# Kernel optimization log

Hardware: AMD Instinct MI355X
Metric: run time of the kernel (lower is better)

## Reference

```python
import jax, jax.numpy as jnp
import numpy as np

N_NODES = 100000
C = 128
E = 800000
V = 50000
NEG_SLOPE = 0.2


def gat_conv(x, edges, W, att_src, att_dst, bias, num_nodes):
    """Single-head PyG-style GATConv with self-loops added (PyG default).

    edges: [2, E] with row 0 = source j, row 1 = destination i.
    """
    loops = jnp.arange(num_nodes, dtype=edges.dtype)
    src = jnp.concatenate([edges[0], loops])  # [E+N]
    dst = jnp.concatenate([edges[1], loops])

    h = x @ W.T                               # [N, C] linear transform
    a_s = h @ att_src                         # [N] per-node src score
    a_d = h @ att_dst                         # [N] per-node dst score

    e = jax.nn.leaky_relu(a_s[src] + a_d[dst], NEG_SLOPE)  # [E+N]
    # scatter-softmax over edges grouped by destination node
    m = jax.ops.segment_max(e, dst, num_segments=num_nodes)
    ex = jnp.exp(e - m[dst])
    denom = jax.ops.segment_sum(ex, dst, num_segments=num_nodes)
    alpha = ex / (denom[dst] + 1e-16)         # [E+N]

    out = jax.ops.segment_sum(alpha[:, None] * h[src], dst, num_segments=num_nodes)
    return out + bias


def setup_inputs() -> dict:
    key = jax.random.key(0)
    ks = jax.random.split(key, 12)
    s = 1.0 / np.sqrt(C)
    return {
        "embedding": jax.random.normal(ks[0], (N_NODES, C), jnp.float32),
        "W1": jax.random.normal(ks[1], (C, C), jnp.float32) * s,
        "att_src1": jax.random.normal(ks[2], (C,), jnp.float32) * s,
        "att_dst1": jax.random.normal(ks[3], (C,), jnp.float32) * s,
        "b1": jax.random.normal(ks[4], (C,), jnp.float32) * s,
        "W2": jax.random.normal(ks[5], (C, C), jnp.float32) * s,
        "att_src2": jax.random.normal(ks[6], (C,), jnp.float32) * s,
        "att_dst2": jax.random.normal(ks[7], (C,), jnp.float32) * s,
        "b2": jax.random.normal(ks[8], (C,), jnp.float32) * s,
        "edges1": jax.random.randint(ks[9], (2, E), 0, N_NODES, jnp.int64 if jax.config.jax_enable_x64 else jnp.int32),
        "edges2": jax.random.randint(ks[10], (2, E), 0, N_NODES, jnp.int64 if jax.config.jax_enable_x64 else jnp.int32),
        "idx_mapping": jax.random.randint(ks[11], (V,), 0, N_NODES, jnp.int64 if jax.config.jax_enable_x64 else jnp.int32),
    }


def reference(embedding, W1, att_src1, att_dst1, b1, W2, att_src2, att_dst2, b2,
              edges1, edges2, idx_mapping):
    h = gat_conv(embedding, edges1, W1, att_src1, att_dst1, b1, N_NODES)
    h = gat_conv(h, edges2, W2, att_src2, att_dst2, b2, N_NODES)
    return h[idx_mapping]
```

## Files before the change

### kernel.cpp

```cpp
#include <hip/hip_runtime.h>

#define N_NODES 100000
#define C_DIM 128
#define E_EDGES 800000
#define V_OUT 50000
#define EN (E_EDGES + N_NODES)
#define M2 (2 * N_NODES)
#define EN2 (2 * EN)

#define BSHIFT 9
#define NBUCK_L ((N_NODES + 511) >> 9)
#define NBUCK2 (2 * NBUCK_L)
#define CAP 8192
#define P1_CHUNK 4096
#define P1_PER_T (P1_CHUNK / 256)
#define NCHUNK ((EN2 + P1_CHUNK - 1) / P1_CHUNK)
#define VFLAG_BLKS ((V_OUT + 255) / 256)

#define XPAD 136
#define LDS_E 768

#define NCHUNKS_G ((N_NODES + 63) / 64)
#define GEMM_GRID 512

typedef unsigned int uint;
typedef unsigned short ushort;
typedef __attribute__((ext_vector_type(8))) short bf16x8;
typedef __attribute__((ext_vector_type(4))) float f32x4;

static __device__ __forceinline__ ushort f2bf(float f) {
    uint u = __float_as_uint(f);
    u += 0x7fffu + ((u >> 16) & 1);
    return (ushort)(u >> 16);
}

template <int IN_F32>
__global__ __launch_bounds__(256) void gemm_mfma(
    const void* __restrict__ xin, const float* __restrict__ W,
    const float* __restrict__ att_s, const float* __restrict__ att_d,
    ushort* __restrict__ hb, float* __restrict__ a_s, float* __restrict__ a_d)
{
    __shared__ ushort ws[128 * XPAD];
    __shared__ ushort xs[2][64 * XPAD];
    const int tid = threadIdx.x;

    {
        const int row = tid >> 1, half = tid & 1;
        const float* src = W + row * 128 + half * 64;
        ushort* dst = &ws[row * XPAD + half * 64];
        #pragma unroll
        for (int i = 0; i < 8; ++i) {
            float4 u = *reinterpret_cast<const float4*>(src + i * 8);
            float4 v = *reinterpret_cast<const float4*>(src + i * 8 + 4);
            uint4 pk;
            pk.x = (uint)f2bf(u.x) | ((uint)f2bf(u.y) << 16);
            pk.y = (uint)f2bf(u.z) | ((uint)f2bf(u.w) << 16);
            pk.z = (uint)f2bf(v.x) | ((uint)f2bf(v.y) << 16);
            pk.w = (uint)f2bf(v.z) | ((uint)f2bf(v.w) << 16);
            *reinterpret_cast<uint4*>(dst + i * 8) = pk;
        }
    }

    const int srow_t = tid >> 2, q = tid & 3;
    const int lane = tid & 63, wv = tid >> 6;
    const int m = lane & 15, quad = lane >> 4;

    int c = blockIdx.x;
    float4 pf_f[8];
    uint4  pf_b[4];

    {
        const long srow = min((long)c * 64 + srow_t, (long)N_NODES - 1);
        if (IN_F32) {
            const float* src = (const float*)xin + srow * 128 + q * 32;
            #pragma unroll
            for (int i = 0; i < 8; ++i)
                pf_f[i] = *reinterpret_cast<const float4*>(src + i * 4);
        } else {
            const ushort* src = (const ushort*)xin + srow * 128 + q * 32;
            #pragma unroll
            for (int i = 0; i < 4; ++i)
                pf_b[i] = *reinterpret_cast<const uint4*>(src + i * 8);
        }
        ushort* dst = &xs[0][srow_t * XPAD + q * 32];
        if (IN_F32) {
            #pragma unroll
            for (int i = 0; i < 4; ++i) {
                uint4 pk;
                pk.x = (uint)f2bf(pf_f[2*i].x)   | ((uint)f2bf(pf_f[2*i].y)   << 16);
                pk.y = (uint)f2bf(pf_f[2*i].z)   | ((uint)f2bf(pf_f[2*i].w)   << 16);
                pk.z = (uint)f2bf(pf_f[2*i+1].x) | ((uint)f2bf(pf_f[2*i+1].y) << 16);
                pk.w = (uint)f2bf(pf_f[2*i+1].z) | ((uint)f2bf(pf_f[2*i+1].w) << 16);
                *reinterpret_cast<uint4*>(dst + i * 8) = pk;
            }
        } else {
            #pragma unroll
            for (int i = 0; i < 4; ++i)
                *reinterpret_cast<uint4*>(dst + i * 8) = pf_b[i];
        }
    }
    __syncthreads();

    int cur = 0;
    while (c < NCHUNKS_G) {
        const int cn = c + GEMM_GRID;

        if (cn < NCHUNKS_G) {
            const long srow = min((long)cn * 64 + srow_t, (long)N_NODES - 1);
            if (IN_F32) {
                const float* src = (const float*)xin + srow * 128 + q * 32;
                #pragma unroll
                for (int i = 0; i < 8; ++i)
                    pf_f[i] = *reinterpret_cast<const float4*>(src + i * 4);
            } else {
                const ushort* src = (const ushort*)xin + srow * 128 + q * 32;
                #pragma unroll
                for (int i = 0; i < 4; ++i)
                    pf_b[i] = *reinterpret_cast<const uint4*>(src + i * 8);
            }
        }

        const int n0 = c * 64 + wv * 16;
        bf16x8 a[4];
        #pragma unroll
        for (int ki = 0; ki < 4; ++ki)
            a[ki] = *reinterpret_cast<const bf16x8*>(&xs[cur][(wv*16+m)*XPAD + quad*8 + ki*32]);
        __syncthreads();

        float ps[4] = {0, 0, 0, 0}, pd[4] = {0, 0, 0, 0};
        #pragma unroll
        for (int ct = 0; ct < 8; ++ct) {
            const int cc = ct * 16 + m;
            f32x4 acc = {0.f, 0.f, 0.f, 0.f};
            #pragma unroll
            for (int ki = 0; ki < 4; ++ki) {
                bf16x8 b = *reinterpret_cast<const bf16x8*>(&ws[cc*XPAD + quad*8 + ki*32]);
                acc = __builtin_amdgcn_mfma_f32_16x16x32_bf16(a[ki], b, acc, 0, 0, 0);
            }
            const float asc = att_s[cc], adc = att_d[cc];
            #pragma unroll
            for (int r = 0; r < 4; ++r) {
                xs[cur][(wv*16 + quad*4 + r) * XPAD + cc] = f2bf(acc[r]);
                ps[r] = fmaf(acc[r], asc, ps[r]);
                pd[r] = fmaf(acc[r], adc, pd[r]);
            }
        }
        __syncthreads();

        {
            const int sub = tid & 15, rb = tid >> 4;
            #pragma unroll
            for (int i = 0; i < 4; ++i) {
                const int rl = rb + i * 16;
                const int node = c * 64 + rl;
                uint4 v = *reinterpret_cast<const uint4*>(&xs[cur][rl * XPAD + sub * 8]);
                if (node < N_NODES)
                    *reinterpret_cast<uint4*>(hb + (long)node * 128 + sub * 8) = v;
            }
        }
        #pragma unroll
        for (int r = 0; r < 4; ++r) {
            float s = ps[r], d = pd[r];
            #pragma unroll
            for (int x = 1; x < 16; x <<= 1) { s += __shfl_xor(s, x); d += __shfl_xor(d, x); }
            const int node = n0 + quad * 4 + r;
            if (m == 0 && node < N_NODES) { a_s[node] = s; a_d[node] = d; }
        }

        if (cn < NCHUNKS_G) {
            ushort* dst = &xs[cur ^ 1][srow_t * XPAD + q * 32];
            if (IN_F32) {
                #pragma unroll
                for (int i = 0; i < 4; ++i) {
                    uint4 pk;
                    pk.x = (uint)f2bf(pf_f[2*i].x)   | ((uint)f2bf(pf_f[2*i].y)   << 16);
                    pk.y = (uint)f2bf(pf_f[2*i].z)   | ((uint)f2bf(pf_f[2*i].w)   << 16);
                    pk.z = (uint)f2bf(pf_f[2*i+1].x) | ((uint)f2bf(pf_f[2*i+1].y) << 16);
                    pk.w = (uint)f2bf(pf_f[2*i+1].z) | ((uint)f2bf(pf_f[2*i+1].w) << 16);
                    *reinterpret_cast<uint4*>(dst + i * 8) = pk;
                }
            } else {
                #pragma unroll
                for (int i = 0; i < 4; ++i)
                    *reinterpret_cast<uint4*>(dst + i * 8) = pf_b[i];
            }
        }
        __syncthreads();
        cur ^= 1;
        c = cn;
    }
}

__global__ __launch_bounds__(256) void partition_kernel(
    const int* __restrict__ e1, const int* __restrict__ e2,
    int* __restrict__ cursor, uint* __restrict__ slab,
    const int* __restrict__ idxm, int* __restrict__ head, int* __restrict__ nextp)
{
    __shared__ int cnt[NBUCK2];
    __shared__ int basearr[NBUCK2];
    const int tid = threadIdx.x;
    const int blk = blockIdx.x;
    if (blk >= NCHUNK) {
        int v = (blk - NCHUNK) * 256 + tid;
        if (v < V_OUT) {
            int n = idxm[v];
            int old = atomicExch(&head[n], v);
            nextp[v] = old;
        }
        return;
    }
    for (int i = tid; i < NBUCK2; i += 256) cnt[i] = 0;
    __syncthreads();

    const int e0 = blk * P1_CHUNK;
    uint ent[P1_PER_T];
    int  bkt[P1_PER_T];
    #pragma unroll
    for (int i = 0; i < P1_PER_T; ++i) {
        int e = e0 + i * 256 + tid;
        bkt[i] = -1;
        if (e < EN2) {
            int src, dst, lb;
            if (e < EN) {
                if (e < E_EDGES) { src = e1[e]; dst = e1[E_EDGES + e]; }
                else             { src = dst = e - E_EDGES; }
                lb = 0;
            } else {
                int f = e - EN;
                if (f < E_EDGES) { src = e2[f]; dst = e2[E_EDGES + f]; }
                else             { src = dst = f - E_EDGES; }
                lb = NBUCK_L;
            }
            bkt[i] = lb + (dst >> BSHIFT);
            ent[i] = (uint)src | ((uint)(dst & 511) << 17);
            atomicAdd(&cnt[bkt[i]], 1);
        }
    }
    __syncthreads();
    for (int b = tid; b < NBUCK2; b += 256) {
        int c = cnt[b];
        basearr[b] = (c > 0) ? atomicAdd(&cursor[b], c) : 0;
        cnt[b] = 0;
    }
    __syncthreads();
    #pragma unroll
    for (int i = 0; i < P1_PER_T; ++i) {
        if (bkt[i] >= 0) {
            int r = basearr[bkt[i]] + atomicAdd(&cnt[bkt[i]], 1);
            if (r < CAP) slab[(long)bkt[i] * CAP + r] = ent[i];
        }
    }
}

__global__ __launch_bounds__(256) void local_csr(
    const uint* __restrict__ slab, const int* __restrict__ cursor,
    int* __restrict__ offs, uint* __restrict__ esrc)
{
    __shared__ uint ent[CAP];
    __shared__ int deg[512];
    __shared__ int excl[512];
    __shared__ int sbase;
    const int b = blockIdx.x;
    const int tid = threadIdx.x;
    const int cnt = min(cursor[b], CAP);
    const int layer = (b >= NBUCK_L);
    const int node0 = (b - layer * NBUCK_L) << BSHIFT;
    const int obase = layer * N_NODES;
    const int nodes_n = min(512, N_NODES - node0);

    for (int i = tid; i < 512; i += 256) deg[i] = 0;
    if (tid < 64) {
        int s = 0;
        #pragma unroll
        for (int k = 0; k < 7; ++k) {
            int idx = tid + 64 * k;
            if (idx < b) s += cursor[idx];
        }
        #pragma unroll
        for (int d = 32; d > 0; d >>= 1) s += __shfl_down(s, d);
        if (tid == 0) sbase = s;
    }
    __syncthreads();
    const int base = sbase;

    for (int i = tid; i < cnt; i += 256) {
        uint v = slab[(long)b * CAP + i];
        ent[i] = v;
        atomicAdd(&deg[v >> 17], 1);
    }
    __syncthreads();
    if (tid < 64) {
        int v8[8]; int s = 0;
        #pragma unroll
        for (int i = 0; i < 8; ++i) { v8[i] = deg[tid * 8 + i]; s += v8[i]; }
        int incl = s;
        #pragma unroll
        for (int d = 1; d < 64; d <<= 1) {
            int t = __shfl_up(incl, d);
            if (tid >= d) incl += t;
        }
        int e = incl - s;
        #pragma unroll
        for (int i = 0; i < 8; ++i) { excl[tid * 8 + i] = e; e += v8[i]; }
    }
    __syncthreads();
    for (int i = tid; i < nodes_n; i += 256)
        offs[obase + node0 + i] = base + excl[i];
    for (int i = tid; i < 512; i += 256) deg[i] = 0;
    if (tid == 0 && node0 + 512 >= N_NODES)
        offs[obase + N_NODES] = base + cnt;
    __syncthreads();
    for (int i = tid; i < cnt; i += 256) {
        uint v = ent[i];
        int dl = v >> 17;
        int r = atomicAdd(&deg[dl], 1);
        esrc[base + excl[dl] + r] = v;
    }
}

template <int MODE>
__global__ __launch_bounds__(256) void aggregate(
    const ushort* __restrict__ hb, const float* __restrict__ a_s,
    const float* __restrict__ a_d, const float* __restrict__ bias,
    const int* __restrict__ offs, const uint* __restrict__ esrc,
    const int* __restrict__ head, const int* __restrict__ nextp,
    void* __restrict__ outp, int obase)
{
    __shared__ uint2 ew[LDS_E];
    const int tid = threadIdx.x;
    const int node0 = blockIdx.x * 16;
    const int bnode0 = (node0 >> BSHIFT) << BSHIFT;
    const int bstart = offs[obase + node0];
    const int bend   = offs[obase + node0 + 16];
    const int nE = bend - bstart;

    for (int i = tid; i < min(nE, LDS_E); i += 256) {
        uint v = esrc[bstart + i];
        float w = 0.0f;
        const int d = bnode0 + (v >> 17);
        if (MODE == 0 || head[d] >= 0) {
            float e = a_s[v & 0x1ffff] + a_d[d];
            e = (e >= 0.0f) ? e : 0.2f * e;
            w = __expf(e);
        }
        ew[i] = make_uint2(v, __float_as_uint(w));
    }
    __syncthreads();

    const int wave = tid >> 6;
    const int lane = tid & 63;
    const int slot = lane >> 4;
    const int c16  = lane & 15;
    const int node = node0 + wave * 4 + slot;
    int hv = 0;
    if (MODE == 1) {
        hv = head[node];
        if (hv < 0) return;
    }

    const int start = offs[obase + node];
    const int end   = offs[obase + node + 1];
    const long coff = (long)(c16 << 3);
    float acc[8] = {0, 0, 0, 0, 0, 0, 0, 0};
    float dsum = 0.0f;

    if (start < end) {
        if (nE <= LDS_E) {
            const int jr = start - bstart, jend = end - bstart;
            const int e1 = jend - 1;
            uint2 p0 = ew[jr];
            uint2 p1 = ew[min(jr + 1, e1)];
            uint2 p2 = ew[min(jr + 2, e1)];
            uint2 p3 = ew[min(jr + 3, e1)];
            uint4 h0 = *reinterpret_cast<const uint4*>(hb + ((long)(p0.x & 0x1ffff) << 7) + coff);
            uint4 h1 = *reinterpret_cast<const uint4*>(hb + ((long)(p1.x & 0x1ffff) << 7) + coff);
            uint4 h2 = *reinterpret_cast<const uint4*>(hb + ((long)(p2.x & 0x1ffff) << 7) + coff);
            uint4 h3 = *reinterpret_cast<const uint4*>(hb + ((long)(p3.x & 0x1ffff) << 7) + coff);
            float w0 = __uint_as_float(p0.y);
            float w1 = __uint_as_float(p1.y);
            float w2 = __uint_as_float(p2.y);
            float w3 = __uint_as_float(p3.y);
            for (int j = jr; j < jend; ++j) {
                uint2 p4 = ew[min(j + 4, e1)];
                uint4 h4 = *reinterpret_cast<const uint4*>(hb + ((long)(p4.x & 0x1ffff) << 7) + coff);
                float w4 = __uint_as_float(p4.y);
                dsum += w0;
                acc[0] = fmaf(w0, __uint_as_float(h0.x << 16),         acc[0]);
                acc[1] = fmaf(w0, __uint_as_float(h0.x & 0xffff0000u), acc[1]);
                acc[2] = fmaf(w0, __uint_as_float(h0.y << 16),         acc[2]);
                acc[3] = fmaf(w0, __uint_as_float(h0.y & 0xffff0000u), acc[3]);
                acc[4] = fmaf(w0, __uint_as_float(h0.z << 16),         acc[4]);
                acc[5] = fmaf(w0, __uint_as_float(h0.z & 0xffff0000u), acc[5]);
                acc[6] = fmaf(w0, __uint_as_float(h0.w << 16),         acc[6]);
                acc[7] = fmaf(w0, __uint_as_float(h0.w & 0xffff0000u), acc[7]);
                w0 = w1; w1 = w2; w2 = w3; w3 = w4;
                h0 = h1; h1 = h2; h2 = h3; h3 = h4;
            }
        } else {
            const float ad = a_d[node];
            for (int j = start; j < end; ++j) {
                uint v = esrc[j];
                float e = a_s[v & 0x1ffff] + ad;
                e = (e >= 0.0f) ? e : 0.2f * e;
                float w = __expf(e);
                uint4 h = *reinterpret_cast<const uint4*>(hb + ((long)(v & 0x1ffff) << 7) + coff);
                dsum += w;
                acc[0] = fmaf(w, __uint_as_float(h.x << 16),         acc[0]);
                acc[1] = fmaf(w, __uint_as_float(h.x & 0xffff0000u), acc[1]);
                acc[2] = fmaf(w, __uint_as_float(h.y << 16),         acc[2]);
                acc[3] = fmaf(w, __uint_as_float(h.y & 0xffff0000u), acc[3]);
                acc[4] = fmaf(w, __uint_as_float(h.z << 16),         acc[4]);
                acc[5] = fmaf(w, __uint_as_float(h.z & 0xffff0000u), acc[5]);
                acc[6] = fmaf(w, __uint_as_float(h.w << 16),         acc[6]);
                acc[7] = fmaf(w, __uint_as_float(h.w & 0xffff0000u), acc[7]);
            }
        }
    }

    const float inv = 1.0f / (dsum + 1e-16f);
    const int c0 = c16 << 3;
    const float4 b0 = *reinterpret_cast<const float4*>(bias + c0);
    const float4 b1 = *reinterpret_cast<const float4*>(bias + c0 + 4);
    float res[8];
    res[0] = fmaf(acc[0], inv, b0.x);
    res[1] = fmaf(acc[1], inv, b0.y);
    res[2] = fmaf(acc[2], inv, b0.z);
    res[3] = fmaf(acc[3], inv, b0.w);
    res[4] = fmaf(acc[4], inv, b1.x);
    res[5] = fmaf(acc[5], inv, b1.y);
    res[6] = fmaf(acc[6], inv, b1.z);
    res[7] = fmaf(acc[7], inv, b1.w);
    if (MODE == 0) {
        uint4 pk;
        pk.x = (uint)f2bf(res[0]) | ((uint)f2bf(res[1]) << 16);
        pk.y = (uint)f2bf(res[2]) | ((uint)f2bf(res[3]) << 16);
        pk.z = (uint)f2bf(res[4]) | ((uint)f2bf(res[5]) << 16);
        pk.w = (uint)f2bf(res[6]) | ((uint)f2bf(res[7]) << 16);
        *reinterpret_cast<uint4*>((ushort*)outp + ((long)node << 7) + c0) = pk;
    } else {
        const float4 r0 = make_float4(res[0], res[1], res[2], res[3]);
        const float4 r1 = make_float4(res[4], res[5], res[6], res[7]);
        for (int v = hv; v >= 0; v = nextp[v]) {
            float* op = (float*)outp + ((long)v << 7) + c0;
            *reinterpret_cast<float4*>(op)     = r0;
            *reinterpret_cast<float4*>(op + 4) = r1;
        }
    }
}

extern "C" void kernel_launch(void* const* d_in, const int* in_sizes, int n_in,
                              void* d_out, int out_size, void* d_ws, size_t ws_size,
                              hipStream_t stream)
{
    const float* emb = (const float*)d_in[0];
    const float* W1  = (const float*)d_in[1];
    const float* as1 = (const float*)d_in[2];
    const float* ad1 = (const float*)d_in[3];
    const float* b1  = (const float*)d_in[4];
    const float* W2  = (const float*)d_in[5];
    const float* as2 = (const float*)d_in[6];
    const float* ad2 = (const float*)d_in[7];
    const float* b2  = (const float*)d_in[8];
    const int* edges1 = (const int*)d_in[9];
    const int* edges2 = (const int*)d_in[10];
    const int* idxm   = (const int*)d_in[11];
    float* out = (float*)d_out;

    char* p = (char*)d_ws;
    auto alloc = [&](size_t bytes) {
        char* r = p;
        p += (bytes + 255) & ~(size_t)255;
        return r;
    };
    ushort* hb   = (ushort*)alloc((size_t)N_NODES * C_DIM * 2);
    ushort* a1o  = (ushort*)alloc((size_t)N_NODES * C_DIM * 2);
    uint*   slab = (uint*)alloc((size_t)NBUCK2 * CAP * 4);
    uint*   esrc = (uint*)alloc((size_t)EN2 * 4);
    int*    offs = (int*)alloc((size_t)(M2 + 1) * 4);
    float*  aS   = (float*)alloc((size_t)N_NODES * 4);
    float*  aD   = (float*)alloc((size_t)N_NODES * 4);
    int*  cursor = (int*)alloc((size_t)NBUCK2 * 4);
    int*  head   = (int*)alloc((size_t)N_NODES * 4);
    int*  nextp  = (int*)alloc((size_t)V_OUT * 4);

    hipMemsetAsync(cursor, 0, (size_t)NBUCK2 * 4, stream);
    hipMemsetAsync(head, 0xFF, (size_t)N_NODES * 4, stream);

    partition_kernel<<<NCHUNK + VFLAG_BLKS, 256, 0, stream>>>(
        edges1, edges2, cursor, slab, idxm, head, nextp);
    local_csr<<<NBUCK2, 256, 0, stream>>>(slab, cursor, offs, esrc);

    gemm_mfma<1><<<GEMM_GRID, 256, 0, stream>>>(emb, W1, as1, ad1, hb, aS, aD);
    aggregate<0><<<N_NODES / 16, 256, 0, stream>>>(hb, aS, aD, b1, offs, esrc, head, nextp, a1o, 0);

    gemm_mfma<0><<<GEMM_GRID, 256, 0, stream>>>(a1o, W2, as2, ad2, hb, aS, aD);
    aggregate<1><<<N_NODES / 16, 256, 0, stream>>>(hb, aS, aD, b2, offs, esrc, head, nextp, out, N_NODES);
}
```

Measured before the change: 266.9 us.

## Replace persistent double-buffered GEMM with one-tile-per-block, direct register A loads

The GEMM kernel drops its persistent grid-stride loop with a double-buffered LDS staging tile for X. Each block now handles one 64-row tile, loads the A fragments straight from global memory into registers, and reuses the W shared buffer to stage the bf16 output. Removing the xs buffer cuts shared memory per block, and launch bounds of 4 blocks per CU aim for higher occupancy in place of explicit prefetch. The trade-offs are that W is reloaded and converted by every one of the ~1563 blocks, and global loads are no longer overlapped by software pipelining.

New measurement: 271.2 us. No clear change (+1.6%).

```diff
diff --git a/kernel.cpp b/kernel.cpp
--- a/kernel.cpp
+++ b/kernel.cpp
@@ -20,9 +20,6 @@
 #define XPAD 136
 #define LDS_E 768
 
-#define NCHUNKS_G ((N_NODES + 63) / 64)
-#define GEMM_GRID 512
-
 typedef unsigned int uint;
 typedef unsigned short ushort;
 typedef __attribute__((ext_vector_type(8))) short bf16x8;
@@ -35,13 +32,12 @@
 }
 
 template <int IN_F32>
-__global__ __launch_bounds__(256) void gemm_mfma(
+__global__ __launch_bounds__(256, 4) void gemm_mfma(
     const void* __restrict__ xin, const float* __restrict__ W,
     const float* __restrict__ att_s, const float* __restrict__ att_d,
     ushort* __restrict__ hb, float* __restrict__ a_s, float* __restrict__ a_d)
 {
     __shared__ ushort ws[128 * XPAD];
-    __shared__ ushort xs[2][64 * XPAD];
     const int tid = threadIdx.x;
 
     {
@@ -61,133 +57,86 @@
         }
     }
 
-    const int srow_t = tid >> 2, q = tid & 3;
     const int lane = tid & 63, wv = tid >> 6;
     const int m = lane & 15, quad = lane >> 4;
-
-    int c = blockIdx.x;
-    float4 pf_f[8];
-    uint4  pf_b[4];
+    const int nb = blockIdx.x * 64;
+    const int n0 = nb + wv * 16;
+    const long xrow = min((long)(n0 + m), (long)N_NODES - 1);
+
+    bf16x8 a[4];
+    if (IN_F32) {
+        const float* src = (const float*)xin + xrow * 128 + quad * 8;
+        #pragma unroll
+        for (int ki = 0; ki < 4; ++ki) {
+            float4 u = *reinterpret_cast<const float4*>(src + ki * 32);
+            float4 v = *reinterpret_cast<const float4*>(src + ki * 32 + 4);
+            uint4 pk;
+            pk.x = (uint)f2bf(u.x) | ((uint)f2bf(u.y) << 16);
+            pk.y = (uint)f2bf(u.z) | ((uint)f2bf(u.w) << 16);
+            pk.z = (uint)f2bf(v.x) | ((uint)f2bf(v.y) << 16);
+            pk.w = (uint)f2bf(v.z) | ((uint)f2bf(v.w) << 16);
+            a[ki] = *reinterpret_cast<bf16x8*>(&pk);
+        }
+    } else {
+        const ushort* src = (const ushort*)xin + xrow * 128 + quad * 8;
+        #pragma unroll
+        for (int ki = 0; ki < 4; ++ki)
+            a[ki] = *reinterpret_cast<const bf16x8*>(src + ki * 32);
+    }
+    __syncthreads();
+
+    float ps[4] = {0, 0, 0, 0}, pd[4] = {0, 0, 0, 0};
+    uint2 packed[8];
+    #pragma unroll
+    for (int ct = 0; ct < 8; ++ct) {
+        const int cc = ct * 16 + m;
+        f32x4 acc = {0.f, 0.f, 0.f, 0.f};
+        #pragma unroll
+        for (int ki = 0; ki < 4; ++ki) {
+            bf16x8 b = *reinterpret_cast<const bf16x8*>(&ws[cc * XPAD + quad * 8 + ki * 32]);
+            acc = __builtin_amdgcn_mfma_f32_16x16x32_bf16(a[ki], b, acc, 0, 0, 0);
+        }
+        const float asc = att_s[cc], adc = att_d[cc];
+        #pragma unroll
+        for (int r = 0; r < 4; ++r) {
+            ps[r] = fmaf(acc[r], asc, ps[r]);
+            pd[r] = fmaf(acc[r], adc, pd[r]);
+        }
+        packed[ct].x = (uint)f2bf(acc[0]) | ((uint)f2bf(acc[1]) << 16);
+        packed[ct].y = (uint)f2bf(acc[2]) | ((uint)f2bf(acc[3]) << 16);
+    }
+    __syncthreads();
 
     {
-        const long srow = min((long)c * 64 + srow_t, (long)N_NODES - 1);
-        if (IN_F32) {
-            const float* src = (const float*)xin + srow * 128 + q * 32;
-            #pragma unroll
-            for (int i = 0; i < 8; ++i)
-                pf_f[i] = *reinterpret_cast<const float4*>(src + i * 4);
-        } else {
-            const ushort* src = (const ushort*)xin + srow * 128 + q * 32;
-            #pragma unroll
-            for (int i = 0; i < 4; ++i)
-                pf_b[i] = *reinterpret_cast<const uint4*>(src + i * 8);
-        }
-        ushort* dst = &xs[0][srow_t * XPAD + q * 32];
-        if (IN_F32) {
-            #pragma unroll
-            for (int i = 0; i < 4; ++i) {
-                uint4 pk;
-                pk.x = (uint)f2bf(pf_f[2*i].x)   | ((uint)f2bf(pf_f[2*i].y)   << 16);
-                pk.y = (uint)f2bf(pf_f[2*i].z)   | ((uint)f2bf(pf_f[2*i].w)   << 16);
-                pk.z = (uint)f2bf(pf_f[2*i+1].x) | ((uint)f2bf(pf_f[2*i+1].y) << 16);
-                pk.w = (uint)f2bf(pf_f[2*i+1].z) | ((uint)f2bf(pf_f[2*i+1].w) << 16);
-                *reinterpret_cast<uint4*>(dst + i * 8) = pk;
-            }
-        } else {
-            #pragma unroll
-            for (int i = 0; i < 4; ++i)
-                *reinterpret_cast<uint4*>(dst + i * 8) = pf_b[i];
-        }
-    }
-    __syncthreads();
-
-    int cur = 0;
-    while (c < NCHUNKS_G) {
-        const int cn = c + GEMM_GRID;
-
-        if (cn < NCHUNKS_G) {
-            const long srow = min((long)cn * 64 + srow_t, (long)N_NODES - 1);
-            if (IN_F32) {
-                const float* src = (const float*)xin + srow * 128 + q * 32;
-                #pragma unroll
-                for (int i = 0; i < 8; ++i)
-                    pf_f[i] = *reinterpret_cast<const float4*>(src + i * 4);
-            } else {
-                const ushort* src = (const ushort*)xin + srow * 128 + q * 32;
-                #pragma unroll
-                for (int i = 0; i < 4; ++i)
-                    pf_b[i] = *reinterpret_cast<const uint4*>(src + i * 8);
-            }
-        }
-
-        const int n0 = c * 64 + wv * 16;
-        bf16x8 a[4];
-        #pragma unroll
-        for (int ki = 0; ki < 4; ++ki)
-            a[ki] = *reinterpret_cast<const bf16x8*>(&xs[cur][(wv*16+m)*XPAD + quad*8 + ki*32]);
-        __syncthreads();
-
-        float ps[4] = {0, 0, 0, 0}, pd[4] = {0, 0, 0, 0};
+        const int rowb = (wv * 16 + quad * 4) * XPAD + m;
         #pragma unroll
         for (int ct = 0; ct < 8; ++ct) {
-            const int cc = ct * 16 + m;
-            f32x4 acc = {0.f, 0.f, 0.f, 0.f};
-            #pragma unroll
-            for (int ki = 0; ki < 4; ++ki) {
-                bf16x8 b = *reinterpret_cast<const bf16x8*>(&ws[cc*XPAD + quad*8 + ki*32]);
-                acc = __builtin_amdgcn_mfma_f32_16x16x32_bf16(a[ki], b, acc, 0, 0, 0);
-            }
-            const float asc = att_s[cc], adc = att_d[cc];
-            #pragma unroll
-            for (int r = 0; r < 4; ++r) {
-                xs[cur][(wv*16 + quad*4 + r) * XPAD + cc] = f2bf(acc[r]);
-                ps[r] = fmaf(acc[r], asc, ps[r]);
-                pd[r] = fmaf(acc[r], adc, pd[r]);
-            }
-        }
-        __syncthreads();
-
-        {
-            const int sub = tid & 15, rb = tid >> 4;
-            #pragma unroll
-            for (int i = 0; i < 4; ++i) {
-                const int rl = rb + i * 16;
-                const int node = c * 64 + rl;
-                uint4 v = *reinterpret_cast<const uint4*>(&xs[cur][rl * XPAD + sub * 8]);
-                if (node < N_NODES)
-                    *reinterpret_cast<uint4*>(hb + (long)node * 128 + sub * 8) = v;
-            }
-        }
-        #pragma unroll
-        for (int r = 0; r < 4; ++r) {
-            float s = ps[r], d = pd[r];
-            #pragma unroll
-            for (int x = 1; x < 16; x <<= 1) { s += __shfl_xor(s, x); d += __shfl_xor(d, x); }
-            const int node = n0 + quad * 4 + r;
-            if (m == 0 && node < N_NODES) { a_s[node] = s; a_d[node] = d; }
-        }
-
-        if (cn < NCHUNKS_G) {
-            ushort* dst = &xs[cur ^ 1][srow_t * XPAD + q * 32];
-            if (IN_F32) {
-                #pragma unroll
-                for (int i = 0; i < 4; ++i) {
-                    uint4 pk;
-                    pk.x = (uint)f2bf(pf_f[2*i].x)   | ((uint)f2bf(pf_f[2*i].y)   << 16);
-                    pk.y = (uint)f2bf(pf_f[2*i].z)   | ((uint)f2bf(pf_f[2*i].w)   << 16);
-                    pk.z = (uint)f2bf(pf_f[2*i+1].x) | ((uint)f2bf(pf_f[2*i+1].y) << 16);
-                    pk.w = (uint)f2bf(pf_f[2*i+1].z) | ((uint)f2bf(pf_f[2*i+1].w) << 16);
-                    *reinterpret_cast<uint4*>(dst + i * 8) = pk;
-                }
-            } else {
-                #pragma unroll
-                for (int i = 0; i < 4; ++i)
-                    *reinterpret_cast<uint4*>(dst + i * 8) = pf_b[i];
-            }
-        }
-        __syncthreads();
-        cur ^= 1;
-        c = cn;
+            ws[rowb            + ct * 16] = (ushort)(packed[ct].x);
+            ws[rowb +     XPAD + ct * 16] = (ushort)(packed[ct].x >> 16);
+            ws[rowb + 2 * XPAD + ct * 16] = (ushort)(packed[ct].y);
+            ws[rowb + 3 * XPAD + ct * 16] = (ushort)(packed[ct].y >> 16);
+        }
+    }
+    __syncthreads();
+
+    {
+        const int sub = tid & 15, rb = tid >> 4;
+        #pragma unroll
+        for (int i = 0; i < 4; ++i) {
+            const int rl = rb + i * 16;
+            const int node = nb + rl;
+            uint4 v = *reinterpret_cast<const uint4*>(&ws[rl * XPAD + sub * 8]);
+            if (node < N_NODES)
+                *reinterpret_cast<uint4*>(hb + (long)node * 128 + sub * 8) = v;
+        }
+    }
+    #pragma unroll
+    for (int r = 0; r < 4; ++r) {
+        float s = ps[r], d = pd[r];
+        #pragma unroll
+        for (int x = 1; x < 16; x <<= 1) { s += __shfl_xor(s, x); d += __shfl_xor(d, x); }
+        const int node = n0 + quad * 4 + r;
+        if (m == 0 && node < N_NODES) { a_s[node] = s; a_d[node] = d; }
     }
 }
 
@@ -490,9 +439,9 @@
         edges1, edges2, cursor, slab, idxm, head, nextp);
     local_csr<<<NBUCK2, 256, 0, stream>>>(slab, cursor, offs, esrc);
 
-    gemm_mfma<1><<<GEMM_GRID, 256, 0, stream>>>(emb, W1, as1, ad1, hb, aS, aD);
+    gemm_mfma<1><<<(N_NODES + 63) / 64, 256, 0, stream>>>(emb, W1, as1, ad1, hb, aS, aD);
     aggregate<0><<<N_NODES / 16, 256, 0, stream>>>(hb, aS, aD, b1, offs, esrc, head, nextp, a1o, 0);
 
-    gemm_mfma<0><<<GEMM_GRID, 256, 0, stream>>>(a1o, W2, as2, ad2, hb, aS, aD);
+    gemm_mfma<0><<<(N_NODES + 63) / 64, 256, 0, stream>>>(a1o, W2, as2, ad2, hb, aS, aD);
     aggregate<1><<<N_NODES / 16, 256, 0, stream>>>(hb, aS, aD, b2, offs, esrc, head, nextp, out, N_NODES);
 }
```
